# Performance work log

Measured on AMD Instinct MI355X. Metric: run time of the kernel, lower is better.

Reference implementation:

```python
import jax, jax.numpy as jnp
import numpy as np

N, F_IN, H, F_OUT, E = 50000, 128, 8, 16, 800000


def setup_inputs() -> dict:
    key = jax.random.key(0)
    ks = jax.random.split(key, 10)
    x = jax.random.normal(ks[0], (N, F_IN), dtype=jnp.float32)
    edge_index = jax.random.randint(ks[1], (2, E), 0, N, dtype=jnp.int64 if jax.config.read('jax_enable_x64') else jnp.int32)
    edge_prob = jax.random.uniform(ks[2], (E, 1), dtype=jnp.float32)
    s = 1.0 / np.sqrt(F_IN)
    Wp = jax.random.normal(ks[3], (H * F_OUT, F_IN), dtype=jnp.float32) * s
    Wt = jax.random.normal(ks[4], (H * F_OUT, 1), dtype=jnp.float32)
    a_src = jax.random.normal(ks[5], (H, F_OUT), dtype=jnp.float32) * 0.1
    a_trg = jax.random.normal(ks[6], (H, F_OUT), dtype=jnp.float32) * 0.1
    a_tp = jax.random.normal(ks[7], (H, F_OUT), dtype=jnp.float32) * 0.1
    Wskip = jax.random.normal(ks[8], (H * F_OUT, F_IN), dtype=jnp.float32) * s
    bias = jnp.zeros((H * F_OUT,), dtype=jnp.float32)
    return {"x": x, "edge_index": edge_index, "edge_prob": edge_prob,
            "Wp": Wp, "Wt": Wt, "a_src": a_src, "a_trg": a_trg,
            "a_tp": a_tp, "Wskip": Wskip, "bias": bias}


def reference(x, edge_index, edge_prob, Wp, Wt, a_src, a_trg, a_tp, Wskip, bias):
    n = x.shape[0]
    h, f = a_src.shape
    src, trg = edge_index[0], edge_index[1]
    # node projection: [N, H, F_out]
    proj = (x @ Wp.T).reshape(n, h, f)
    # transition-prob projection: [E, H, F_out]
    trans = (edge_prob @ Wt.T).reshape(-1, h, f)
    # per-node source/target scores [N, H], per-edge prob score [E, H]
    s_src = jnp.einsum('nhf,hf->nh', proj, a_src)
    s_trg = jnp.einsum('nhf,hf->nh', proj, a_trg)
    s_tp = jnp.einsum('ehf,hf->eh', trans, a_tp)
    scores = jax.nn.leaky_relu(s_src[src] + s_trg[trg] + s_tp, negative_slope=0.2)
    # global-max-shifted exp, segment softmax over target nodes
    e = jnp.exp(scores - jnp.max(scores))
    denom = jax.ops.segment_sum(e, trg, num_segments=n)
    attn = e / (denom[trg] + 1e-16)  # [E, H]
    weighted = proj[src] * attn[..., None]  # [E, H, F_out]
    out = jax.ops.segment_sum(weighted, trg, num_segments=n)  # [N, H, F_out]
    # skip connection (F_out != F_in -> skip_proj path), concat heads, bias, ELU
    out = out + (x @ Wskip.T).reshape(n, h, f)
    out = out.reshape(n, h * f) + bias
    return jax.nn.elu(out)
```

## Files before the change

kernel.cpp:

```cpp
#include <hip/hip_runtime.h>
#include <hip/hip_fp16.h>
#include <math.h>

constexpr int Nn  = 50000;
constexpr int FIN = 128;
constexpr int NH  = 8;
constexpr int FO  = 16;
constexpr int HF  = 128;
constexpr int NWR = 272;
constexpr int NPREP = NWR / 2;
constexpr int NBLK64 = (Nn + 63) / 64;
constexpr int NSCAN = (Nn + 255) / 256;

typedef _Float16 f16x8 __attribute__((ext_vector_type(8)));
typedef float    f32x4 __attribute__((ext_vector_type(4)));

__global__ __launch_bounds__(256) void k_pc(
    const float* __restrict__ Wp, const float* __restrict__ Wskip,
    const float* __restrict__ a_src, const float* __restrict__ a_trg,
    const float* __restrict__ Wt, const float* __restrict__ a_tp,
    _Float16* __restrict__ Wh, float* __restrict__ ctp,
    const int* __restrict__ trg, int* __restrict__ deg,
    int* __restrict__ rank, int E)
{
    const int bid = blockIdx.x;
    if (bid < NPREP) {
        if (bid == 0 && threadIdx.x < NH) {
            int h = threadIdx.x;
            float s = 0.f;
            #pragma unroll
            for (int f = 0; f < FO; ++f) s += Wt[h * FO + f] * a_tp[h * FO + f];
            ctp[h] = s;
        }
        const int o = bid * 2 + (threadIdx.x >> 7);
        const int k = threadIdx.x & 127;
        float v;
        if (o < 128)      v = Wp[o * FIN + k];
        else if (o < 256) v = Wskip[(o - 128) * FIN + k];
        else if (o < 264) {
            const int h = o - 256;
            float s = 0.f;
            #pragma unroll
            for (int f = 0; f < FO; ++f)
                s += a_src[h * FO + f] * Wp[(h * FO + f) * FIN + k];
            v = s;
        } else {
            const int h = o - 264;
            float s = 0.f;
            #pragma unroll
            for (int f = 0; f < FO; ++f)
                s += a_trg[h * FO + f] * Wp[(h * FO + f) * FIN + k];
            v = s;
        }
        Wh[o * FIN + k] = (_Float16)v;
        return;
    }

    int e = (bid - NPREP) * 256 + threadIdx.x;
    if (e < E) rank[e] = atomicAdd(&deg[trg[e]], 1);
}

__global__ __launch_bounds__(256) void k_scan1(const int* __restrict__ deg,
                                               int* __restrict__ partial)
{
    __shared__ int lds[256];
    int t = threadIdx.x, i = blockIdx.x * 256 + t;
    lds[t] = (i < Nn) ? deg[i] : 0;
    __syncthreads();
    for (int off = 128; off > 0; off >>= 1) {
        if (t < off) lds[t] += lds[t + off];
        __syncthreads();
    }
    if (t == 0) partial[blockIdx.x] = lds[0];
}

__global__ __launch_bounds__(256) void k_scan3(const int* __restrict__ deg,
                                               const int* __restrict__ partial,
                                               int* __restrict__ pos)
{
    __shared__ int lds[256], lds2[256];
    const int t = threadIdx.x;
    const int i = blockIdx.x * 256 + t;
    lds2[t] = (t < NSCAN) ? partial[t] : 0;
    __syncthreads();
    for (int off = 1; off < 256; off <<= 1) {
        int u = (t >= off) ? lds2[t - off] : 0;
        __syncthreads();
        lds2[t] += u;
        __syncthreads();
    }
    const int base = (blockIdx.x == 0) ? 0 : lds2[blockIdx.x - 1];
    int v = (i < Nn) ? deg[i] : 0;
    lds[t] = v;
    __syncthreads();
    for (int off = 1; off < 256; off <<= 1) {
        int u = (t >= off) ? lds[t - off] : 0;
        __syncthreads();
        lds[t] += u;
        __syncthreads();
    }
    if (i < Nn) pos[i] = base + lds[t] - v;
}

__global__ __launch_bounds__(256) void k_fn(
    const int* __restrict__ src, const int* __restrict__ trg,
    const float* __restrict__ prob, const int* __restrict__ rank,
    const int* __restrict__ pos, unsigned int* __restrict__ spk,
    const float* __restrict__ x, const _Float16* __restrict__ Wh,
    const float* __restrict__ bias,
    __half* __restrict__ projA, float* __restrict__ out,
    float* __restrict__ ssrc, float* __restrict__ strg_s, int E, int nbFill)
{
    const int bid = blockIdx.x;

    if (bid < nbFill) {
        int e4 = bid * 256 + threadIdx.x;
        if (e4 * 4 < E) {
            int4   s4 = reinterpret_cast<const int4*>(src)[e4];
            int4   t4 = reinterpret_cast<const int4*>(trg)[e4];
            float4 p4 = reinterpret_cast<const float4*>(prob)[e4];
            int4   r4 = reinterpret_cast<const int4*>(rank)[e4];
            int    sv[4] = {s4.x, s4.y, s4.z, s4.w};
            int    tv[4] = {t4.x, t4.y, t4.z, t4.w};
            int    rv[4] = {r4.x, r4.y, r4.z, r4.w};
            float  pv[4] = {p4.x, p4.y, p4.z, p4.w};
            #pragma unroll
            for (int i = 0; i < 4; ++i) {
                int slot = pos[tv[i]] + rv[i];
                spk[slot] = (unsigned int)sv[i] |
                    ((unsigned int)__half_as_ushort(__float2half_rn(pv[i])) << 16);
            }
        }
        return;
    }

    const int g0 = (bid - nbFill) * 64;
    const int w  = threadIdx.x >> 6;
    const int l  = threadIdx.x & 63;
    const int lr = l & 15;
    const int kb = l >> 4;
    const int t0 = w * 4;

    f16x8 b[4][4];
    const _Float16* wb = Wh + (size_t)lr * FIN + kb * 8;
    #pragma unroll
    for (int i = 0; i < 4; ++i) {
        #pragma unroll
        for (int ks = 0; ks < 4; ++ks)
            b[i][ks] = *reinterpret_cast<const f16x8*>(
                wb + (size_t)(t0 + i) * 16 * FIN + ks * 32);
    }
    f16x8 b16[4];
    if (w == 3) {
        #pragma unroll
        for (int ks = 0; ks < 4; ++ks)
            b16[ks] = *reinterpret_cast<const f16x8*>(
                wb + (size_t)16 * 16 * FIN + ks * 32);
    }

    const float* xr0 = x + (size_t)(g0 + lr) * FIN + kb * 8;

    if (g0 + 64 <= Nn) {
        float4 ucur[8];
        #pragma unroll
        for (int q = 0; q < 8; ++q)
            ucur[q] = *reinterpret_cast<const float4*>(
                xr0 + (q >> 1) * 32 + (q & 1) * 4);

        #pragma unroll
        for (int ng = 0; ng < 4; ++ng) {
            float4 unx[8];
            if (ng < 3) {
                const float* xrn = xr0 + (size_t)(ng + 1) * 16 * FIN;
                #pragma unroll
                for (int q = 0; q < 8; ++q)
                    unx[q] = *reinterpret_cast<const float4*>(
                        xrn + (q >> 1) * 32 + (q & 1) * 4);
            }

            f16x8 a[4];
            #pragma unroll
            for (int ks = 0; ks < 4; ++ks) {
                float4 lo = ucur[ks * 2], hi = ucur[ks * 2 + 1];
                a[ks][0] = (_Float16)lo.x; a[ks][1] = (_Float16)lo.y;
                a[ks][2] = (_Float16)lo.z; a[ks][3] = (_Float16)lo.w;
                a[ks][4] = (_Float16)hi.x; a[ks][5] = (_Float16)hi.y;
                a[ks][6] = (_Float16)hi.z; a[ks][7] = (_Float16)hi.w;
            }

            f32x4 acc[4];
            #pragma unroll
            for (int i = 0; i < 4; ++i) acc[i] = (f32x4){0.f, 0.f, 0.f, 0.f};
            f32x4 acc16 = (f32x4){0.f, 0.f, 0.f, 0.f};

            #pragma unroll
            for (int i = 0; i < 4; ++i) {
                #pragma unroll
                for (int ks = 0; ks < 4; ++ks)
                    acc[i] = __builtin_amdgcn_mfma_f32_16x16x32_f16(
                        a[ks], b[i][ks], acc[i], 0, 0, 0);
            }
            if (w == 3) {
                #pragma unroll
                for (int ks = 0; ks < 4; ++ks)
                    acc16 = __builtin_amdgcn_mfma_f32_16x16x32_f16(
                        a[ks], b16[ks], acc16, 0, 0, 0);
            }

            const int n0 = g0 + ng * 16;
            #pragma unroll
            for (int r = 0; r < 4; ++r) {
                const int n = n0 + kb * 4 + r;
                if (t0 < 8) {
                    #pragma unroll
                    for (int i = 0; i < 4; ++i)
                        projA[(size_t)n * HF + (t0 + i) * FO + lr] =
                            __float2half_rn(acc[i][r]);
                } else {
                    #pragma unroll
                    for (int i = 0; i < 4; ++i) {
                        const int o = (t0 + i - 8) * 16 + lr;
                        out[(size_t)n * HF + o] = acc[i][r] + bias[o];
                    }
                }
                if (w == 3) {
                    if (lr < 8) ssrc[n * 8 + lr] = acc16[r];
                    else        strg_s[n * 8 + (lr - 8)] = acc16[r];
                }
            }

            #pragma unroll
            for (int q = 0; q < 8; ++q) ucur[q] = unx[q];
        }
    } else {
        f16x8 a[4];
        #pragma unroll
        for (int ks = 0; ks < 4; ++ks) {
            float4 u0 = *reinterpret_cast<const float4*>(xr0 + ks * 32);
            float4 u1 = *reinterpret_cast<const float4*>(xr0 + ks * 32 + 4);
            a[ks][0] = (_Float16)u0.x; a[ks][1] = (_Float16)u0.y;
            a[ks][2] = (_Float16)u0.z; a[ks][3] = (_Float16)u0.w;
            a[ks][4] = (_Float16)u1.x; a[ks][5] = (_Float16)u1.y;
            a[ks][6] = (_Float16)u1.z; a[ks][7] = (_Float16)u1.w;
        }

        f32x4 acc[4];
        #pragma unroll
        for (int i = 0; i < 4; ++i) acc[i] = (f32x4){0.f, 0.f, 0.f, 0.f};
        f32x4 acc16 = (f32x4){0.f, 0.f, 0.f, 0.f};

        #pragma unroll
        for (int i = 0; i < 4; ++i) {
            #pragma unroll
            for (int ks = 0; ks < 4; ++ks)
                acc[i] = __builtin_amdgcn_mfma_f32_16x16x32_f16(
                    a[ks], b[i][ks], acc[i], 0, 0, 0);
        }
        if (w == 3) {
            #pragma unroll
            for (int ks = 0; ks < 4; ++ks)
                acc16 = __builtin_amdgcn_mfma_f32_16x16x32_f16(
                    a[ks], b16[ks], acc16, 0, 0, 0);
        }

        #pragma unroll
        for (int r = 0; r < 4; ++r) {
            const int n = g0 + kb * 4 + r;
            if (t0 < 8) {
                #pragma unroll
                for (int i = 0; i < 4; ++i)
                    projA[(size_t)n * HF + (t0 + i) * FO + lr] =
                        __float2half_rn(acc[i][r]);
            } else {
                #pragma unroll
                for (int i = 0; i < 4; ++i) {
                    const int o = (t0 + i - 8) * 16 + lr;
                    out[(size_t)n * HF + o] = acc[i][r] + bias[o];
                }
            }
            if (w == 3) {
                if (lr < 8) ssrc[n * 8 + lr] = acc16[r];
                else        strg_s[n * 8 + (lr - 8)] = acc16[r];
            }
        }
    }
}

__global__ __launch_bounds__(256) void k_gather(
    const unsigned int* __restrict__ spk, const int* __restrict__ pos,
    const float* __restrict__ ssrc, const float* __restrict__ strg_s,
    const float* __restrict__ ctp,
    const __half2* __restrict__ projA, float* __restrict__ out, int E)
{
    const int lane = threadIdx.x & 63;
    const int h    = lane >> 3;
    const int f2   = lane & 7;

    const int n = __builtin_amdgcn_readfirstlane(
        blockIdx.x * 4 + (threadIdx.x >> 6));

    const int jb = __builtin_amdgcn_readfirstlane(pos[n]);
    const int je = __builtin_amdgcn_readfirstlane((n + 1 < Nn) ? pos[n + 1] : E);

    const float st  = strg_s[n * 8 + h];
    const float cth = ctp[h];
    const float* __restrict__ ssl = ssrc + h;
    const __half2* __restrict__ pA = projA + h * 8 + f2;

    float num0 = 0.f, num1 = 0.f, den = 0.f;
    int j = jb;
    for (; j + 3 < je; j += 4) {
        const unsigned int pk0 = __builtin_amdgcn_readfirstlane(spk[j]);
        const unsigned int pk1 = __builtin_amdgcn_readfirstlane(spk[j + 1]);
        const unsigned int pk2 = __builtin_amdgcn_readfirstlane(spk[j + 2]);
        const unsigned int pk3 = __builtin_amdgcn_readfirstlane(spk[j + 3]);
        const int s0 = pk0 & 0xFFFF, s1 = pk1 & 0xFFFF;
        const int s2 = pk2 & 0xFFFF, s3 = pk3 & 0xFFFF;
        const float ss0 = ssl[s0 * 8], ss1 = ssl[s1 * 8];
        const float ss2 = ssl[s2 * 8], ss3 = ssl[s3 * 8];
        const __half2 g0 = pA[s0 * 64], g1 = pA[s1 * 64];
        const __half2 g2 = pA[s2 * 64], g3 = pA[s3 * 64];
        const float p0 = __half2float(__ushort_as_half((unsigned short)(pk0 >> 16)));
        const float p1 = __half2float(__ushort_as_half((unsigned short)(pk1 >> 16)));
        const float p2 = __half2float(__ushort_as_half((unsigned short)(pk2 >> 16)));
        const float p3 = __half2float(__ushort_as_half((unsigned short)(pk3 >> 16)));
        float sc0 = ss0 + st + cth * p0;
        float sc1 = ss1 + st + cth * p1;
        float sc2 = ss2 + st + cth * p2;
        float sc3 = ss3 + st + cth * p3;
        sc0 = fmaxf(sc0, 0.2f * sc0);
        sc1 = fmaxf(sc1, 0.2f * sc1);
        sc2 = fmaxf(sc2, 0.2f * sc2);
        sc3 = fmaxf(sc3, 0.2f * sc3);
        const float ev0 = __expf(sc0), ev1 = __expf(sc1);
        const float ev2 = __expf(sc2), ev3 = __expf(sc3);
        const float2 G0 = __half22float2(g0), G1 = __half22float2(g1);
        const float2 G2 = __half22float2(g2), G3 = __half22float2(g3);
        den  += (ev0 + ev1) + (ev2 + ev3);
        num0 += ev0 * G0.x + ev1 * G1.x + ev2 * G2.x + ev3 * G3.x;
        num1 += ev0 * G0.y + ev1 * G1.y + ev2 * G2.y + ev3 * G3.y;
    }
    for (; j < je; ++j) {
        const unsigned int pk = __builtin_amdgcn_readfirstlane(spk[j]);
        const int s = pk & 0xFFFF;
        const float p = __half2float(__ushort_as_half((unsigned short)(pk >> 16)));
        float sc = ssl[s * 8] + st + cth * p;
        sc = fmaxf(sc, 0.2f * sc);
        const float ev = __expf(sc);
        const float2 G = __half22float2(pA[s * 64]);
        den  += ev;
        num0 += ev * G.x;
        num1 += ev * G.y;
    }

    const float inv = 1.f / (den + 1e-16f);
    const int idx = n * HF + h * FO + f2 * 2;
    float2 o = *reinterpret_cast<const float2*>(&out[idx]);
    float v0 = o.x + num0 * inv;
    float v1 = o.y + num1 * inv;
    v0 = v0 > 0.f ? v0 : expm1f(v0);
    v1 = v1 > 0.f ? v1 : expm1f(v1);
    *reinterpret_cast<float2*>(&out[idx]) = make_float2(v0, v1);
}

extern "C" void kernel_launch(void* const* d_in, const int* in_sizes, int n_in,
                              void* d_out, int out_size, void* d_ws, size_t ws_size,
                              hipStream_t stream)
{
    const float* x     = (const float*)d_in[0];
    const int*   ei    = (const int*)d_in[1];
    const float* prob  = (const float*)d_in[2];
    const float* Wp    = (const float*)d_in[3];
    const float* Wt    = (const float*)d_in[4];
    const float* a_src = (const float*)d_in[5];
    const float* a_trg = (const float*)d_in[6];
    const float* a_tp  = (const float*)d_in[7];
    const float* Wskip = (const float*)d_in[8];
    const float* bias  = (const float*)d_in[9];
    float* out = (float*)d_out;

    const int E = in_sizes[2];
    const int* src = ei;
    const int* trg = ei + E;

    char* wsb = (char*)d_ws;
    __half* projA  = (__half*)wsb;
    float* ssrc    = (float*)(wsb + (size_t)Nn*HF*2);
    float* strg_s  = ssrc + (size_t)Nn * 8;
    float* ctp     = strg_s + (size_t)Nn * 8;
    _Float16* Wh   = (_Float16*)(ctp + 16);
    unsigned int* spk = (unsigned int*)(Wh + (size_t)NWR * FIN);
    int*   rank    = (int*)(spk + E);
    int*   deg     = rank + E;
    int*   pos     = deg + Nn;
    int*   partial = pos + Nn;

    const int nbCount = (E + 255) / 256;
    const int nbFill  = (E + 1023) / 1024;

    hipMemsetAsync(deg, 0, (size_t)Nn * sizeof(int), stream);
    k_pc<<<NPREP + nbCount, 256, 0, stream>>>(Wp, Wskip, a_src, a_trg, Wt,
                                              a_tp, Wh, ctp, trg, deg, rank, E);
    k_scan1<<<NSCAN, 256, 0, stream>>>(deg, partial);
    k_scan3<<<NSCAN, 256, 0, stream>>>(deg, partial, pos);
    k_fn<<<nbFill + NBLK64, 256, 0, stream>>>(src, trg, prob, rank, pos, spk,
                                              x, Wh, bias, projA, out,
                                              ssrc, strg_s, E, nbFill);
    k_gather<<<Nn / 4, 256, 0, stream>>>(spk, pos, ssrc, strg_s, ctp,
                                         (const __half2*)projA, out, E);
}
```

Before: 133.8 us.

## Fuse degree counting into the node GEMM kernel and split CSR fill

Edge degree counting with atomics moves out of the weight-prep kernel and into the node-projection GEMM kernel, which runs the atomics after its matrix work. Each thread now counts four edges with vectorized trg loads. The CSR fill becomes its own kernel that runs after the scans. The intent is to overlap the atomic-bound counting with the compute-bound projection, at the cost of one extra launch and a serial prep kernel.

```diff
diff --git a/kernel.cpp b/kernel.cpp
--- a/kernel.cpp
+++ b/kernel.cpp
@@ -8,133 +8,63 @@
 constexpr int FO  = 16;
 constexpr int HF  = 128;
 constexpr int NWR = 272;
-constexpr int NPREP = NWR / 2;
 constexpr int NBLK64 = (Nn + 63) / 64;
 constexpr int NSCAN = (Nn + 255) / 256;
 
 typedef _Float16 f16x8 __attribute__((ext_vector_type(8)));
 typedef float    f32x4 __attribute__((ext_vector_type(4)));
 
-__global__ __launch_bounds__(256) void k_pc(
+__global__ __launch_bounds__(256) void k_prep(
     const float* __restrict__ Wp, const float* __restrict__ Wskip,
     const float* __restrict__ a_src, const float* __restrict__ a_trg,
     const float* __restrict__ Wt, const float* __restrict__ a_tp,
-    _Float16* __restrict__ Wh, float* __restrict__ ctp,
-    const int* __restrict__ trg, int* __restrict__ deg,
-    int* __restrict__ rank, int E)
-{
-    const int bid = blockIdx.x;
-    if (bid < NPREP) {
-        if (bid == 0 && threadIdx.x < NH) {
-            int h = threadIdx.x;
-            float s = 0.f;
-            #pragma unroll
-            for (int f = 0; f < FO; ++f) s += Wt[h * FO + f] * a_tp[h * FO + f];
-            ctp[h] = s;
-        }
-        const int o = bid * 2 + (threadIdx.x >> 7);
-        const int k = threadIdx.x & 127;
-        float v;
-        if (o < 128)      v = Wp[o * FIN + k];
-        else if (o < 256) v = Wskip[(o - 128) * FIN + k];
-        else if (o < 264) {
-            const int h = o - 256;
-            float s = 0.f;
-            #pragma unroll
-            for (int f = 0; f < FO; ++f)
-                s += a_src[h * FO + f] * Wp[(h * FO + f) * FIN + k];
-            v = s;
-        } else {
-            const int h = o - 264;
-            float s = 0.f;
-            #pragma unroll
-            for (int f = 0; f < FO; ++f)
-                s += a_trg[h * FO + f] * Wp[(h * FO + f) * FIN + k];
-            v = s;
-        }
-        Wh[o * FIN + k] = (_Float16)v;
-        return;
-    }
-
-    int e = (bid - NPREP) * 256 + threadIdx.x;
-    if (e < E) rank[e] = atomicAdd(&deg[trg[e]], 1);
-}
-
-__global__ __launch_bounds__(256) void k_scan1(const int* __restrict__ deg,
-                                               int* __restrict__ partial)
-{
-    __shared__ int lds[256];
-    int t = threadIdx.x, i = blockIdx.x * 256 + t;
-    lds[t] = (i < Nn) ? deg[i] : 0;
-    __syncthreads();
-    for (int off = 128; off > 0; off >>= 1) {
-        if (t < off) lds[t] += lds[t + off];
-        __syncthreads();
-    }
-    if (t == 0) partial[blockIdx.x] = lds[0];
-}
-
-__global__ __launch_bounds__(256) void k_scan3(const int* __restrict__ deg,
-                                               const int* __restrict__ partial,
-                                               int* __restrict__ pos)
-{
-    __shared__ int lds[256], lds2[256];
-    const int t = threadIdx.x;
-    const int i = blockIdx.x * 256 + t;
-    lds2[t] = (t < NSCAN) ? partial[t] : 0;
-    __syncthreads();
-    for (int off = 1; off < 256; off <<= 1) {
-        int u = (t >= off) ? lds2[t - off] : 0;
-        __syncthreads();
-        lds2[t] += u;
-        __syncthreads();
-    }
-    const int base = (blockIdx.x == 0) ? 0 : lds2[blockIdx.x - 1];
-    int v = (i < Nn) ? deg[i] : 0;
-    lds[t] = v;
-    __syncthreads();
-    for (int off = 1; off < 256; off <<= 1) {
-        int u = (t >= off) ? lds[t - off] : 0;
-        __syncthreads();
-        lds[t] += u;
-        __syncthreads();
-    }
-    if (i < Nn) pos[i] = base + lds[t] - v;
-}
-
-__global__ __launch_bounds__(256) void k_fn(
-    const int* __restrict__ src, const int* __restrict__ trg,
-    const float* __restrict__ prob, const int* __restrict__ rank,
-    const int* __restrict__ pos, unsigned int* __restrict__ spk,
+    _Float16* __restrict__ Wh, float* __restrict__ ctp)
+{
+    if (blockIdx.x == 0 && threadIdx.x < NH) {
+        int h = threadIdx.x;
+        float s = 0.f;
+        #pragma unroll
+        for (int f = 0; f < FO; ++f) s += Wt[h * FO + f] * a_tp[h * FO + f];
+        ctp[h] = s;
+    }
+    const int o = blockIdx.x * 2 + (threadIdx.x >> 7);
+    const int k = threadIdx.x & 127;
+    float v;
+    if (o < 128)      v = Wp[o * FIN + k];
+    else if (o < 256) v = Wskip[(o - 128) * FIN + k];
+    else if (o < 264) {
+        const int h = o - 256;
+        float s = 0.f;
+        #pragma unroll
+        for (int f = 0; f < FO; ++f)
+            s += a_src[h * FO + f] * Wp[(h * FO + f) * FIN + k];
+        v = s;
+    } else {
+        const int h = o - 264;
+        float s = 0.f;
+        #pragma unroll
+        for (int f = 0; f < FO; ++f)
+            s += a_trg[h * FO + f] * Wp[(h * FO + f) * FIN + k];
+        v = s;
+    }
+    Wh[o * FIN + k] = (_Float16)v;
+}
+
+__global__ __launch_bounds__(256) void k_cn(
+    const int* __restrict__ trg, int* __restrict__ deg, int* __restrict__ rank,
     const float* __restrict__ x, const _Float16* __restrict__ Wh,
     const float* __restrict__ bias,
     __half* __restrict__ projA, float* __restrict__ out,
-    float* __restrict__ ssrc, float* __restrict__ strg_s, int E, int nbFill)
+    float* __restrict__ ssrc, float* __restrict__ strg_s, int E)
 {
     const int bid = blockIdx.x;
 
-    if (bid < nbFill) {
-        int e4 = bid * 256 + threadIdx.x;
-        if (e4 * 4 < E) {
-            int4   s4 = reinterpret_cast<const int4*>(src)[e4];
-            int4   t4 = reinterpret_cast<const int4*>(trg)[e4];
-            float4 p4 = reinterpret_cast<const float4*>(prob)[e4];
-            int4   r4 = reinterpret_cast<const int4*>(rank)[e4];
-            int    sv[4] = {s4.x, s4.y, s4.z, s4.w};
-            int    tv[4] = {t4.x, t4.y, t4.z, t4.w};
-            int    rv[4] = {r4.x, r4.y, r4.z, r4.w};
-            float  pv[4] = {p4.x, p4.y, p4.z, p4.w};
-            #pragma unroll
-            for (int i = 0; i < 4; ++i) {
-                int slot = pos[tv[i]] + rv[i];
-                spk[slot] = (unsigned int)sv[i] |
-                    ((unsigned int)__half_as_ushort(__float2half_rn(pv[i])) << 16);
-            }
-        }
-        return;
-    }
-
-    const int g0 = (bid - nbFill) * 64;
+    const int e4 = bid * 256 + threadIdx.x;
+    const bool doCnt = (e4 * 4 < E);
+    int4 t4;
+    if (doCnt) t4 = reinterpret_cast<const int4*>(trg)[e4];
+
+    const int g0 = bid * 64;
     const int w  = threadIdx.x >> 6;
     const int l  = threadIdx.x & 63;
     const int lr = l & 15;
@@ -283,6 +213,80 @@
                 else        strg_s[n * 8 + (lr - 8)] = acc16[r];
             }
         }
+    }
+
+    if (doCnt) {
+        int4 r;
+        r.x = atomicAdd(&deg[t4.x], 1);
+        r.y = atomicAdd(&deg[t4.y], 1);
+        r.z = atomicAdd(&deg[t4.z], 1);
+        r.w = atomicAdd(&deg[t4.w], 1);
+        reinterpret_cast<int4*>(rank)[e4] = r;
+    }
+}
+
+__global__ __launch_bounds__(256) void k_scan1(const int* __restrict__ deg,
+                                               int* __restrict__ partial)
+{
+    __shared__ int lds[256];
+    int t = threadIdx.x, i = blockIdx.x * 256 + t;
+    lds[t] = (i < Nn) ? deg[i] : 0;
+    __syncthreads();
+    for (int off = 128; off > 0; off >>= 1) {
+        if (t < off) lds[t] += lds[t + off];
+        __syncthreads();
+    }
+    if (t == 0) partial[blockIdx.x] = lds[0];
+}
+
+__global__ __launch_bounds__(256) void k_scan3(const int* __restrict__ deg,
+                                               const int* __restrict__ partial,
+                                               int* __restrict__ pos)
+{
+    __shared__ int lds[256], lds2[256];
+    const int t = threadIdx.x;
+    const int i = blockIdx.x * 256 + t;
+    lds2[t] = (t < NSCAN) ? partial[t] : 0;
+    __syncthreads();
+    for (int off = 1; off < 256; off <<= 1) {
+        int u = (t >= off) ? lds2[t - off] : 0;
+        __syncthreads();
+        lds2[t] += u;
+        __syncthreads();
+    }
+    const int base = (blockIdx.x == 0) ? 0 : lds2[blockIdx.x - 1];
+    int v = (i < Nn) ? deg[i] : 0;
+    lds[t] = v;
+    __syncthreads();
+    for (int off = 1; off < 256; off <<= 1) {
+        int u = (t >= off) ? lds[t - off] : 0;
+        __syncthreads();
+        lds[t] += u;
+        __syncthreads();
+    }
+    if (i < Nn) pos[i] = base + lds[t] - v;
+}
+
+__global__ __launch_bounds__(256) void k_fill(
+    const int* __restrict__ src, const int* __restrict__ trg,
+    const float* __restrict__ prob, const int* __restrict__ rank,
+    const int* __restrict__ pos, unsigned int* __restrict__ spk, int E)
+{
+    int e4 = blockIdx.x * 256 + threadIdx.x;
+    if (e4 * 4 >= E) return;
+    int4   s4 = reinterpret_cast<const int4*>(src)[e4];
+    int4   t4 = reinterpret_cast<const int4*>(trg)[e4];
+    float4 p4 = reinterpret_cast<const float4*>(prob)[e4];
+    int4   r4 = reinterpret_cast<const int4*>(rank)[e4];
+    int    sv[4] = {s4.x, s4.y, s4.z, s4.w};
+    int    tv[4] = {t4.x, t4.y, t4.z, t4.w};
+    int    rv[4] = {r4.x, r4.y, r4.z, r4.w};
+    float  pv[4] = {p4.x, p4.y, p4.z, p4.w};
+    #pragma unroll
+    for (int i = 0; i < 4; ++i) {
+        int slot = pos[tv[i]] + rv[i];
+        spk[slot] = (unsigned int)sv[i] |
+            ((unsigned int)__half_as_ushort(__float2half_rn(pv[i])) << 16);
     }
 }
 
@@ -395,17 +399,14 @@
     int*   pos     = deg + Nn;
     int*   partial = pos + Nn;
 
-    const int nbCount = (E + 255) / 256;
-    const int nbFill  = (E + 1023) / 1024;
-
     hipMemsetAsync(deg, 0, (size_t)Nn * sizeof(int), stream);
-    k_pc<<<NPREP + nbCount, 256, 0, stream>>>(Wp, Wskip, a_src, a_trg, Wt,
-                                              a_tp, Wh, ctp, trg, deg, rank, E);
+    k_prep<<<NWR / 2, 256, 0, stream>>>(Wp, Wskip, a_src, a_trg, Wt, a_tp,
+                                        Wh, ctp);
+    k_cn<<<NBLK64, 256, 0, stream>>>(trg, deg, rank, x, Wh, bias,
+                                     projA, out, ssrc, strg_s, E);
     k_scan1<<<NSCAN, 256, 0, stream>>>(deg, partial);
     k_scan3<<<NSCAN, 256, 0, stream>>>(deg, partial, pos);
-    k_fn<<<nbFill + NBLK64, 256, 0, stream>>>(src, trg, prob, rank, pos, spk,
-                                              x, Wh, bias, projA, out,
-                                              ssrc, strg_s, E, nbFill);
+    k_fill<<<NBLK64, 256, 0, stream>>>(src, trg, prob, rank, pos, spk, E);
     k_gather<<<Nn / 4, 256, 0, stream>>>(spk, pos, ssrc, strg_s, ctp,
                                          (const __half2*)projA, out, E);
 }
```

Result: faster. 127.0 us (-5.1%).
